# Kernel tuning notes

Hardware: AMD Instinct MI355X
Metric: run time of the kernel (lower is better)

The kernel has to match this reference:

```python
import jax, jax.numpy as jnp
import numpy as np

B, S, D, H = 4, 2048, 1024, 16
HD = D // H  # 64


def setup_inputs() -> dict:
    key = jax.random.key(0)
    ks = jax.random.split(key, 11)
    scale = 1.0 / np.sqrt(D)
    inp = {
        "query": jax.random.normal(ks[0], (B, S, D), jnp.float32),
        "key": jax.random.normal(ks[1], (B, S, D), jnp.float32),
        "value": jax.random.normal(ks[2], (B, S, D), jnp.float32),
        "mask": jnp.ones((B, 1, 1, S), jnp.float32),
        "wq": jax.random.normal(ks[3], (D, D), jnp.float32) * scale,
        "bq": jnp.zeros((D,), jnp.float32),
        "wk": jax.random.normal(ks[4], (D, D), jnp.float32) * scale,
        "bk": jnp.zeros((D,), jnp.float32),
        "wv": jax.random.normal(ks[5], (D, D), jnp.float32) * scale,
        "bv": jnp.zeros((D,), jnp.float32),
        "wo": jax.random.normal(ks[6], (D, D), jnp.float32) * scale,
        "bo": jnp.zeros((D,), jnp.float32),
    }
    return inp


def reference(query, key, value, mask, wq, bq, wk, bk, wv, bv, wo, bo):
    b = query.shape[0]
    # Dense QKV projections
    q = query @ wq + bq  # [B,S,D]
    k = key @ wk + bk
    v = value @ wv + bv

    def split_heads(x):
        return x.reshape(b, -1, H, HD).transpose(0, 2, 1, 3)  # [B,H,S,HD]

    q, k, v = split_heads(q), split_heads(k), split_heads(v)
    score = jnp.einsum("bhqd,bhkd->bhqk", q, k) / jnp.sqrt(jnp.float32(HD))
    score = score + (1.0 - mask) * -1e9
    alpha = jax.nn.softmax(score, axis=-1)
    context = jnp.einsum("bhqk,bhkd->bhqd", alpha, v)  # [B,H,S,HD]
    context = context.transpose(0, 2, 1, 3).reshape(b, -1, D)
    return context @ wo + bo
```

## Files before the change

kernel.cpp:

```cpp
#include <hip/hip_runtime.h>

using u16 = unsigned short;
using u32 = unsigned int;

typedef float  f32x4  __attribute__((ext_vector_type(4)));
typedef float  f32x16 __attribute__((ext_vector_type(16)));
typedef u32    u32x4  __attribute__((ext_vector_type(4)));
typedef _Float16 f16;
typedef f16 f16x8 __attribute__((ext_vector_type(8)));

#define DEVI static __device__ __forceinline__

constexpr int S_  = 2048;
constexpr int D_  = 1024;
constexpr int HD_ = 64;
constexpr int SH_ = S_*HD_;
constexpr size_t NE_ = 8192ull*1024ull;

DEVI f32x4 mfma16f(f16x8 a, f16x8 b, f32x4 c){
  return __builtin_amdgcn_mfma_f32_16x16x32_f16(a, b, c, 0, 0, 0);
}
DEVI f32x16 mfma32(f16x8 a, f16x8 b, f32x16 c){
  return __builtin_amdgcn_mfma_f32_32x32x16_f16(a, b, c, 0, 0, 0);
}
DEVI float exp2fast(float x){
#if __has_builtin(__builtin_amdgcn_exp2f)
  return __builtin_amdgcn_exp2f(x);
#else
  float r; asm("v_exp_f32 %0, %1" : "=v"(r) : "v"(x)); return r;
#endif
}
DEVI float rcpfast(float x){
#if __has_builtin(__builtin_amdgcn_rcpf)
  return __builtin_amdgcn_rcpf(x);
#else
  float r; asm("v_rcp_f32 %0, %1" : "=v"(r) : "v"(x)); return r;
#endif
}
DEVI u32 pkh(float a, float b){
  return __builtin_bit_cast(u32, __builtin_amdgcn_cvt_pkrtz(a, b));
}
DEVI void gld16(const void* g, void* l){
  __builtin_amdgcn_global_load_lds(
      (const __attribute__((address_space(1))) u32*)g,
      (__attribute__((address_space(3))) u32*)l, 16, 0, 0);
}
DEVI void gld4(const void* g, void* l){
  __builtin_amdgcn_global_load_lds(
      (const __attribute__((address_space(1))) u32*)g,
      (__attribute__((address_space(3))) u32*)l, 4, 0, 0);
}

__global__ __launch_bounds__(256) void wcvt_k(
    const float* __restrict__ wq, const float* __restrict__ wk,
    const float* __restrict__ wv, const float* __restrict__ wo,
    u16* __restrict__ wt)
{
  int z = blockIdx.z;
  const float* W = (z==0)?wq:(z==1)?wk:(z==2)?wv:wo;
  u16* ot = wt + (size_t)z*D_*D_;
  __shared__ float t[64][65];
  int k0 = blockIdx.y*64, n0 = blockIdx.x*64;
  int tid = threadIdx.x;
#pragma unroll
  for (int i=0;i<4;i++){
    int lin = i*256 + tid;
    int r = lin>>4, c = (lin&15)*4;
    f32x4 v = *reinterpret_cast<const f32x4*>(W + (size_t)(k0+r)*D_ + n0 + c);
    t[r][c+0]=v.x; t[r][c+1]=v.y; t[r][c+2]=v.z; t[r][c+3]=v.w;
  }
  __syncthreads();
  int n = tid>>2, c0 = (tid&3)*16;
  alignas(16) u16 hb[16];
#pragma unroll
  for (int i=0;i<16;i++) hb[i] = __builtin_bit_cast(u16, (f16)t[c0+i][n]);
  size_t off = (size_t)(n0+n)*D_ + k0 + c0;
  *reinterpret_cast<u32x4*>(ot+off)   = *reinterpret_cast<u32x4*>(hb);
  *reinterpret_cast<u32x4*>(ot+off+8) = *reinterpret_cast<u32x4*>(hb+8);
}

__global__ __launch_bounds__(256) void acvt_k(
    const float* __restrict__ q, const float* __restrict__ k,
    const float* __restrict__ v, u16* __restrict__ out)
{
  int z = blockIdx.y;
  const float* src = (z==0)?q:(z==1)?k:v;
  u16* dst = out + (size_t)z*NE_;
  size_t i = ((size_t)blockIdx.x*256 + threadIdx.x)*8;
  f32x4 a = *reinterpret_cast<const f32x4*>(src + i);
  f32x4 b = *reinterpret_cast<const f32x4*>(src + i + 4);
  u32x4 t;
  t.x = pkh(a.x,a.y); t.y = pkh(a.z,a.w);
  t.z = pkh(b.x,b.y); t.w = pkh(b.z,b.w);
  *reinterpret_cast<u32x4*>(dst + i) = t;
}

__global__ __launch_bounds__(256) void madd_k(const float* __restrict__ mask,
                                              float* __restrict__ madd2)
{
  int i = blockIdx.x*256 + threadIdx.x;
  if (i < 4*S_) madd2[i] = (1.0f - mask[i]) * -1442695040.0f;
}

struct GemmArgs {
  const void* A[3];
  const u16*  Wt[3];
  const float* bias[3];
  float*      outF[3];
  u16*        outH[3];
  float       scale[3];
  int         mode[3];
};

__global__ __launch_bounds__(512, 4) void gemm_k(GemmArgs args)
{
  int z = blockIdx.z;
  const u16*   __restrict__ A    = (const u16*)args.A[z];
  const u16*   __restrict__ Wt   = args.Wt[z];
  const float* __restrict__ bias = args.bias[z];
  int mode = args.mode[z];
  float sc = args.scale[z];

  constexpr int ABYT = 16384;
  constexpr int BUFS = ABYT + 8192;
  __shared__ __align__(16) unsigned char smem[73728];
  char* sbase = (char*)smem;

  int m0 = blockIdx.x*256, n0 = blockIdx.y*128;
  int tid = threadIdx.x, lane = tid&63, w = tid>>6;
  int wm = (w>>1)*64, wn = (w&1)*64;
  int lr = lane&15, lh = lane>>4;

  int offA[2], offB;
#pragma unroll
  for (int j=0;j<2;j++){
    int chunk = w*2 + j;
    int row = chunk*16 + (lane>>2);
    int gs = lane&3;
    offA[j] = row*D_ + (((gs - (row>>1)) & 3)*8);
  }
  {
    int row = w*16 + (lane>>2);
    int gs = lane&3;
    offB = row*D_ + (((gs - (row>>1)) & 3)*8);
  }

  f32x4 acc[4][4];
#pragma unroll
  for (int m=0;m<4;m++)
#pragma unroll
    for (int n=0;n<4;n++) acc[m][n] = f32x4{0.f,0.f,0.f,0.f};

  auto STAGE = [&](int buf, int kt){
    char* lA = sbase + buf*BUFS;
    char* lB = lA + ABYT;
    const u16* As = A  + (size_t)m0*D_ + kt*32;
#pragma unroll
    for (int j=0;j<2;j++) gld16(As + offA[j], lA + (w*2+j)*1024);
    const u16* Bs = Wt + (size_t)n0*D_ + kt*32;
    gld16(Bs + offB, lB + w*1024);
  };

  STAGE(0, 0);
  STAGE(1, 1);
  STAGE(2, 2);

  for (int kt=0; kt<32; ++kt){
    int buf = kt - (kt/3)*3;
    if (kt < 30)       asm volatile("s_waitcnt vmcnt(6)" ::: "memory");
    else if (kt == 30) asm volatile("s_waitcnt vmcnt(3)" ::: "memory");
    else               asm volatile("s_waitcnt vmcnt(0)" ::: "memory");
    __builtin_amdgcn_s_barrier();

    char* bA = sbase + buf*BUFS;
    char* bB = bA + ABYT;
    f16x8 af[4], bfr[4];
#pragma unroll
    for (int m=0;m<4;m++){
      int row = wm + m*16 + lr;
      af[m] = *reinterpret_cast<const f16x8*>(bA + row*64 + (((lh + (row>>1)) & 3)<<4));
    }
#pragma unroll
    for (int n=0;n<4;n++){
      int row = wn + n*16 + lr;
      bfr[n] = *reinterpret_cast<const f16x8*>(bB + row*64 + (((lh + (row>>1)) & 3)<<4));
    }
    asm volatile("s_waitcnt lgkmcnt(0)" ::: "memory");
    __builtin_amdgcn_sched_barrier(0);
    __builtin_amdgcn_s_barrier();
    if (kt < 29) STAGE(buf, kt+3);

    __builtin_amdgcn_s_setprio(1);
#pragma unroll
    for (int m=0;m<4;m++)
#pragma unroll
      for (int n=0;n<4;n++)
        acc[m][n] = mfma16f(af[m], bfr[n], acc[m][n]);
    __builtin_amdgcn_s_setprio(0);
  }

  float bsetv[4];
#pragma unroll
  for (int n=0;n<4;n++) bsetv[n] = bias[n0 + wn + n*16 + lr];

  if (mode == 0){
    float* out = args.outF[z];
#pragma unroll
    for (int m=0;m<4;m++)
#pragma unroll
      for (int n=0;n<4;n++)
#pragma unroll
        for (int r=0;r<4;r++){
          int row = m0 + wm + m*16 + lh*4 + r;
          int col = n0 + wn + n*16 + lr;
          out[(size_t)row*D_ + col] = (acc[m][n][r] + bsetv[n])*sc;
        }
  } else if (mode == 1){
    u16* oh = args.outH[z];
#pragma unroll
    for (int m=0;m<4;m++)
#pragma unroll
      for (int n=0;n<4;n++)
#pragma unroll
        for (int r=0;r<4;r++){
          int row = m0 + wm + m*16 + lh*4 + r;
          int col = n0 + wn + n*16 + lr;
          float val = (acc[m][n][r] + bsetv[n])*sc;
          int b = row >> 11, s = row & 2047;
          int hh = col >> 6,  dd = col & 63;
          oh[(size_t)(b*16 + hh)*SH_ + (size_t)s*HD_ + dd] =
              __builtin_bit_cast(u16, (f16)val);
        }
  } else {
    __syncthreads();
    u16* ct = (u16*)sbase;
#pragma unroll
    for (int m=0;m<4;m++)
#pragma unroll
      for (int n=0;n<4;n++)
#pragma unroll
        for (int r=0;r<4;r++){
          int lrow = wm + m*16 + lh*4 + r;
          int lcol = wn + n*16 + lr;
          ct[lrow*132 + lcol] = __builtin_bit_cast(u16, (f16)((acc[m][n][r] + bsetv[n])*sc));
        }
    __syncthreads();
    u16* ovt = args.outH[z];
    int b = m0 >> 11, s0 = m0 & 2047;
    int ch = tid >> 2, quarter = tid & 3;
    int gn = n0 + ch;
    int hh = gn >> 6, dd = gn & 63;
    size_t obase = (size_t)(b*16 + hh)*SH_ + (size_t)dd*S_ + s0 + quarter*64;
#pragma unroll
    for (int i=0;i<8;i++){
      alignas(16) u16 tmp[8];
#pragma unroll
      for (int j=0;j<8;j++) tmp[j] = ct[(quarter*64 + i*8 + j)*132 + ch];
      *reinterpret_cast<u32x4*>(ovt + obase + i*8) = *reinterpret_cast<u32x4*>(tmp);
    }
  }
}

__global__ __launch_bounds__(256, 2) void attn_k(
    const f16* __restrict__ Qf, const f16* __restrict__ Kf,
    const f16* __restrict__ Vt, const float* __restrict__ madd2,
    u16* __restrict__ cf)
{
  constexpr int BUFS = 16640;
  __shared__ __align__(16) unsigned char smem[3*BUFS];
  char* sbase = (char*)smem;

  int flat = blockIdx.x + blockIdx.y*gridDim.x;
  int xcd = flat & 7, ix = flat >> 3;
  int bh = xcd + 8*(ix >> 4);
  int qx = ix & 15;
  int b = bh >> 4, head = bh & 15;

  const f16* Qb = Qf + (size_t)bh*SH_;
  const f16* Kb = Kf + (size_t)bh*SH_;
  const f16* Vb = Vt + (size_t)bh*SH_;
  const float* mb = madd2 + (size_t)b*S_;

  int tid = threadIdx.x, lane = tid&63, w = tid>>6;
  int q31 = lane&31, h = lane>>5;
  int qw = qx*128 + w*32;
  int xorv = (q31&7)<<4;

  f16x8 qb[4];
#pragma unroll
  for (int ks=0;ks<4;ks++)
    qb[ks] = *reinterpret_cast<const f16x8*>(Qb + (size_t)(qw + q31)*HD_ + ks*16 + h*8);

  int offK[2], offV[2];
#pragma unroll
  for (int j=0;j<2;j++){
    int L = (w*2+j)*1024 + lane*16;
    int r = L>>7;
    int dby = (L&127) ^ ((r&7)<<4);
    offK[j] = r*HD_ + (dby>>1);
    offV[j] = r*S_  + (dby>>1);
  }

  u32 one2 = 0x3C003C00u;
  u32x4 onev; onev.x=one2; onev.y=one2; onev.z=one2; onev.w=one2;
  f16x8 vones = __builtin_bit_cast(f16x8, onev);

  f32x16 o[2], ol;
#pragma unroll
  for (int n=0;n<2;n++)
#pragma unroll
    for (int r=0;r<16;r++) o[n][r] = 0.f;
#pragma unroll
  for (int r=0;r<16;r++) ol[r] = 0.f;

  auto STAGE = [&](int buf, int kt){
    int kv0 = kt*64;
    char* sKb = sbase + buf*BUFS;
    char* sVb = sKb + 8192;
    char* sMb = sKb + 16384;
#pragma unroll
    for (int j=0;j<2;j++)
      gld16(Kb + (size_t)kv0*HD_ + offK[j], sKb + (w*2+j)*1024);
#pragma unroll
    for (int j=0;j<2;j++)
      gld16(Vb + kv0 + offV[j], sVb + (w*2+j)*1024);
    gld4(mb + kv0 + lane, sMb);
  };

  STAGE(0, 0);
  STAGE(1, 1);
  STAGE(2, 2);

  for (int kt=0; kt<32; ++kt){
    int buf = kt - (kt/3)*3;
    char* sKb = sbase + buf*BUFS;
    char* sVb = sKb + 8192;
    float* sMb = (float*)(sKb + 16384);

    if (kt < 30)       asm volatile("s_waitcnt vmcnt(10)" ::: "memory");
    else if (kt == 30) asm volatile("s_waitcnt vmcnt(5)"  ::: "memory");
    else               asm volatile("s_waitcnt vmcnt(0)"  ::: "memory");
    __builtin_amdgcn_s_barrier();
    __builtin_amdgcn_sched_barrier(0);

    f32x16 st[2];
#pragma unroll
    for (int n=0;n<2;n++)
#pragma unroll
      for (int r=0;r<16;r++) st[n][r] = 0.f;

    __builtin_amdgcn_s_setprio(1);
#pragma unroll
    for (int n=0;n<2;n++){
      int rb = (n*32 + q31)*128;
#pragma unroll
      for (int ks=0;ks<4;ks++){
        f16x8 ka = *reinterpret_cast<const f16x8*>(sKb + ((rb + ks*32 + h*16) ^ xorv));
        st[n] = mfma32(ka, qb[ks], st[n]);
      }
    }
    __builtin_amdgcn_s_setprio(0);

    float mval = sMb[lane];
    if (__ballot(mval != 0.0f)){
#pragma unroll
      for (int n=0;n<2;n++)
#pragma unroll
        for (int g=0;g<4;g++){
          f32x4 mv = *reinterpret_cast<const f32x4*>(sMb + n*32 + g*8 + h*4);
#pragma unroll
          for (int c=0;c<4;c++) st[n][g*4+c] += mv[c];
        }
    }

#pragma unroll
    for (int n=0;n<2;n++)
#pragma unroll
      for (int r=0;r<16;r++) st[n][r] = exp2fast(st[n][r]);

    f16x8 pa[4];
#pragma unroll
    for (int n=0;n<2;n++){
      u32 x[4], y[4];
#pragma unroll
      for (int T=0;T<4;T++){
        x[T] = pkh(st[n][4*T+0], st[n][4*T+1]);
        y[T] = pkh(st[n][4*T+2], st[n][4*T+3]);
      }
#pragma unroll
      for (int k2=0;k2<2;k2++){
        u32 a0=x[2*k2], b0=x[2*k2+1], a1=y[2*k2], b1=y[2*k2+1];
        asm volatile("v_permlane32_swap_b32 %0, %1" : "+v"(a0), "+v"(b0));
        asm volatile("v_permlane32_swap_b32 %0, %1" : "+v"(a1), "+v"(b1));
        u32x4 wv;
        wv.x = a0;
        wv.y = a1;
        wv.z = b0;
        wv.w = b1;
        pa[2*n+k2] = __builtin_bit_cast(f16x8, wv);
      }
    }

    __builtin_amdgcn_s_setprio(1);
#pragma unroll
    for (int n=0;n<2;n++){
      int rb = (n*32 + q31)*128;
#pragma unroll
      for (int ks=0;ks<4;ks++){
        f16x8 vbf = *reinterpret_cast<const f16x8*>(sVb + ((rb + ks*32 + h*16) ^ xorv));
        o[n] = mfma32(pa[ks], vbf, o[n]);
      }
    }
#pragma unroll
    for (int ks=0;ks<4;ks++)
      ol = mfma32(pa[ks], vones, ol);
    __builtin_amdgcn_s_setprio(0);

    asm volatile("s_waitcnt lgkmcnt(0)" ::: "memory");
    __builtin_amdgcn_s_barrier();
    __builtin_amdgcn_sched_barrier(0);
    if (kt < 29) STAGE(buf, kt+3);
  }

#pragma unroll
  for (int n=0;n<2;n++)
#pragma unroll
    for (int r=0;r<16;r++){
      float inv = rcpfast(ol[r]);
      int s = qw + (r&3) + 8*(r>>2) + 4*h;
      int d = head*HD_ + n*32 + q31;
      cf[((size_t)(b*S_ + s))*D_ + d] = __builtin_bit_cast(u16, (f16)(o[n][r]*inv));
    }
}

extern "C" void kernel_launch(void* const* d_in, const int* in_sizes, int n_in,
                              void* d_out, int out_size, void* d_ws, size_t ws_size,
                              hipStream_t stream)
{
  (void)in_sizes; (void)n_in; (void)out_size;
  const float* query=(const float*)d_in[0];
  const float* key  =(const float*)d_in[1];
  const float* value=(const float*)d_in[2];
  const float* mask =(const float*)d_in[3];
  const float* wq=(const float*)d_in[4];
  const float* bq=(const float*)d_in[5];
  const float* wk=(const float*)d_in[6];
  const float* bk=(const float*)d_in[7];
  const float* wv=(const float*)d_in[8];
  const float* bv=(const float*)d_in[9];
  const float* wo=(const float*)d_in[10];
  const float* bo=(const float*)d_in[11];
  float* out = (float*)d_out;

  const size_t WN = 4ull*1024*1024;
  size_t need = WN*2 + 3*NE_*2 + 3*NE_*2 + NE_*2 + 8192*4;
  if (ws_size < need) return;

  char* ws = (char*)d_ws;
  u16* wt = (u16*)ws;
  u16* aq = wt + WN;
  u16* ak = aq + NE_;
  u16* av = ak + NE_;
  u16* qf = av + NE_;
  u16* kf = qf + NE_;
  u16* vt = kf + NE_;
  u16* cf = vt + NE_;
  float* madd2 = (float*)(cf + NE_);

  const float CSC = 0.18033688011112042f;

  wcvt_k<<<dim3(16,16,4), 256, 0, stream>>>(wq,wk,wv,wo,wt);
  acvt_k<<<dim3(4096,3), 256, 0, stream>>>(query,key,value,aq);
  madd_k<<<dim3(32), 256, 0, stream>>>(mask, madd2);

  GemmArgs ga{};
  ga.A[0]=aq; ga.A[1]=ak; ga.A[2]=av;
  ga.Wt[0]=wt;           ga.Wt[1]=wt+1048576;   ga.Wt[2]=wt+2097152;
  ga.bias[0]=bq; ga.bias[1]=bk; ga.bias[2]=bv;
  ga.scale[0]=CSC; ga.scale[1]=1.0f; ga.scale[2]=1.0f;
  ga.mode[0]=1;  ga.mode[1]=1;  ga.mode[2]=2;
  ga.outH[0]=qf; ga.outH[1]=kf; ga.outH[2]=vt;
  gemm_k<<<dim3(32,8,3), 512, 0, stream>>>(ga);

  attn_k<<<dim3(16,64), 256, 0, stream>>>((const f16*)qf,(const f16*)kf,(const f16*)vt,madd2,cf);

  GemmArgs go{};
  go.A[0]=cf;
  go.Wt[0]=wt+3145728;
  go.bias[0]=bo; go.scale[0]=1.0f; go.mode[0]=0; go.outF[0]=out;
  gemm_k<<<dim3(32,8,1), 512, 0, stream>>>(go);
}
```

Before: 213.7 us.

## Software-pipeline QK^T of next KV tile with softmax/PV of current tile

```diff
diff --git a/kernel.cpp b/kernel.cpp
--- a/kernel.cpp
+++ b/kernel.cpp
@@ -305,6 +305,10 @@
   u32x4 onev; onev.x=one2; onev.y=one2; onev.z=one2; onev.w=one2;
   f16x8 vones = __builtin_bit_cast(f16x8, onev);
 
+  f32x16 z16;
+#pragma unroll
+  for (int r=0;r<16;r++) z16[r] = 0.f;
+
   f32x16 o[2], ol;
 #pragma unroll
   for (int n=0;n<2;n++)
@@ -327,39 +331,36 @@
     gld4(mb + kv0 + lane, sMb);
   };
 
-  STAGE(0, 0);
-  STAGE(1, 1);
-  STAGE(2, 2);
-
-  for (int kt=0; kt<32; ++kt){
-    int buf = kt - (kt/3)*3;
-    char* sKb = sbase + buf*BUFS;
-    char* sVb = sKb + 8192;
-    float* sMb = (float*)(sKb + 16384);
-
-    if (kt < 30)       asm volatile("s_waitcnt vmcnt(10)" ::: "memory");
-    else if (kt == 30) asm volatile("s_waitcnt vmcnt(5)"  ::: "memory");
-    else               asm volatile("s_waitcnt vmcnt(0)"  ::: "memory");
-    __builtin_amdgcn_s_barrier();
-    __builtin_amdgcn_sched_barrier(0);
-
-    f32x16 st[2];
-#pragma unroll
-    for (int n=0;n<2;n++)
-#pragma unroll
-      for (int r=0;r<16;r++) st[n][r] = 0.f;
-
+  auto QK = [&](char* sKb, f32x16 (&st)[2]){
     __builtin_amdgcn_s_setprio(1);
 #pragma unroll
     for (int n=0;n<2;n++){
       int rb = (n*32 + q31)*128;
-#pragma unroll
-      for (int ks=0;ks<4;ks++){
+      f16x8 k0 = *reinterpret_cast<const f16x8*>(sKb + ((rb + h*16) ^ xorv));
+      st[n] = mfma32(k0, qb[0], z16);
+#pragma unroll
+      for (int ks=1;ks<4;ks++){
         f16x8 ka = *reinterpret_cast<const f16x8*>(sKb + ((rb + ks*32 + h*16) ^ xorv));
         st[n] = mfma32(ka, qb[ks], st[n]);
       }
     }
     __builtin_amdgcn_s_setprio(0);
+  };
+
+  auto TILE = [&](int t, f32x16 (&cur)[2], f32x16 (&nxt)[2], bool qknext){
+    int bt = t - (t/3)*3;
+    int bn = (t+1) - ((t+1)/3)*3;
+    char* sKt = sbase + bt*BUFS;
+    char* sVb = sKt + 8192;
+    float* sMb = (float*)(sKt + 16384);
+    char* sKn = sbase + bn*BUFS;
+
+    if (t < 30) asm volatile("s_waitcnt vmcnt(5)" ::: "memory");
+    else        asm volatile("s_waitcnt vmcnt(0)" ::: "memory");
+    __builtin_amdgcn_s_barrier();
+    __builtin_amdgcn_sched_barrier(0);
+
+    if (qknext) QK(sKn, nxt);
 
     float mval = sMb[lane];
     if (__ballot(mval != 0.0f)){
@@ -369,14 +370,14 @@
         for (int g=0;g<4;g++){
           f32x4 mv = *reinterpret_cast<const f32x4*>(sMb + n*32 + g*8 + h*4);
 #pragma unroll
-          for (int c=0;c<4;c++) st[n][g*4+c] += mv[c];
+          for (int c=0;c<4;c++) cur[n][g*4+c] += mv[c];
         }
     }
 
 #pragma unroll
     for (int n=0;n<2;n++)
 #pragma unroll
-      for (int r=0;r<16;r++) st[n][r] = exp2fast(st[n][r]);
+      for (int r=0;r<16;r++) cur[n][r] = exp2fast(cur[n][r]);
 
     f16x8 pa[4];
 #pragma unroll
@@ -384,8 +385,8 @@
       u32 x[4], y[4];
 #pragma unroll
       for (int T=0;T<4;T++){
-        x[T] = pkh(st[n][4*T+0], st[n][4*T+1]);
-        y[T] = pkh(st[n][4*T+2], st[n][4*T+3]);
+        x[T] = pkh(cur[n][4*T+0], cur[n][4*T+1]);
+        y[T] = pkh(cur[n][4*T+2], cur[n][4*T+3]);
       }
 #pragma unroll
       for (int k2=0;k2<2;k2++){
@@ -419,7 +420,24 @@
     asm volatile("s_waitcnt lgkmcnt(0)" ::: "memory");
     __builtin_amdgcn_s_barrier();
     __builtin_amdgcn_sched_barrier(0);
-    if (kt < 29) STAGE(buf, kt+3);
+    if (t <= 28) STAGE(bt, t+3);
+  };
+
+  f32x16 stA[2], stB[2];
+
+  STAGE(0, 0);
+  STAGE(1, 1);
+  STAGE(2, 2);
+
+  asm volatile("s_waitcnt vmcnt(10)" ::: "memory");
+  __builtin_amdgcn_s_barrier();
+  __builtin_amdgcn_sched_barrier(0);
+  QK(sbase, stA);
+
+  for (int i=0;i<16;++i){
+    int u = 2*i, v = 2*i+1;
+    TILE(u, stA, stB, true);
+    TILE(v, stB, stA, v < 31);
   }
 
 #pragma unroll
```

After: 213.6 us. About the same (-0.1%).

## Double-buffer 128-key tiles in attention loop instead of triple-buffered 64-key tiles

Applied to the files above, without the earlier changes.

```diff
diff --git a/kernel.cpp b/kernel.cpp
--- a/kernel.cpp
+++ b/kernel.cpp
@@ -266,8 +266,8 @@
     const f16* __restrict__ Vt, const float* __restrict__ madd2,
     u16* __restrict__ cf)
 {
-  constexpr int BUFS = 16640;
-  __shared__ __align__(16) unsigned char smem[3*BUFS];
+  constexpr int BUFS = 33280;
+  __shared__ __align__(16) unsigned char smem[2*BUFS];
   char* sbase = (char*)smem;
 
   int flat = blockIdx.x + blockIdx.y*gridDim.x;
@@ -291,20 +291,26 @@
   for (int ks=0;ks<4;ks++)
     qb[ks] = *reinterpret_cast<const f16x8*>(Qb + (size_t)(qw + q31)*HD_ + ks*16 + h*8);
 
-  int offK[2], offV[2];
-#pragma unroll
-  for (int j=0;j<2;j++){
-    int L = (w*2+j)*1024 + lane*16;
-    int r = L>>7;
-    int dby = (L&127) ^ ((r&7)<<4);
-    offK[j] = r*HD_ + (dby>>1);
-    offV[j] = r*S_  + (dby>>1);
+  int offK[4], offV[4];
+#pragma unroll
+  for (int j=0;j<4;j++){
+    int L = (w*4+j)*1024 + lane*16;
+    int rK = L>>7;
+    int dbyK = (L&127) ^ ((rK&7)<<4);
+    offK[j] = rK*HD_ + (dbyK>>1);
+    int rV = L>>8;
+    int dbyV = (L&255) ^ ((rV&7)<<4);
+    offV[j] = rV*S_ + (dbyV>>1);
   }
 
   u32 one2 = 0x3C003C00u;
   u32x4 onev; onev.x=one2; onev.y=one2; onev.z=one2; onev.w=one2;
   f16x8 vones = __builtin_bit_cast(f16x8, onev);
 
+  f32x16 z16;
+#pragma unroll
+  for (int r=0;r<16;r++) z16[r] = 0.f;
+
   f32x16 o[2], ol;
 #pragma unroll
   for (int n=0;n<2;n++)
@@ -313,113 +319,125 @@
 #pragma unroll
   for (int r=0;r<16;r++) ol[r] = 0.f;
 
-  auto STAGE = [&](int buf, int kt){
-    int kv0 = kt*64;
+  auto STAGE = [&](int buf, int t){
+    int kv0 = t*128;
     char* sKb = sbase + buf*BUFS;
-    char* sVb = sKb + 8192;
-    char* sMb = sKb + 16384;
-#pragma unroll
-    for (int j=0;j<2;j++)
-      gld16(Kb + (size_t)kv0*HD_ + offK[j], sKb + (w*2+j)*1024);
-#pragma unroll
-    for (int j=0;j<2;j++)
-      gld16(Vb + kv0 + offV[j], sVb + (w*2+j)*1024);
+    char* sVb = sKb + 16384;
+    char* sMb = sKb + 32768;
+#pragma unroll
+    for (int j=0;j<4;j++)
+      gld16(Kb + (size_t)kv0*HD_ + offK[j], sKb + (w*4+j)*1024);
+#pragma unroll
+    for (int j=0;j<4;j++)
+      gld16(Vb + kv0 + offV[j], sVb + (w*4+j)*1024);
     gld4(mb + kv0 + lane, sMb);
+    gld4(mb + kv0 + 64 + lane, sMb + 256);
   };
 
   STAGE(0, 0);
   STAGE(1, 1);
-  STAGE(2, 2);
-
-  for (int kt=0; kt<32; ++kt){
-    int buf = kt - (kt/3)*3;
+
+  for (int t=0; t<16; ++t){
+    int buf = t&1;
     char* sKb = sbase + buf*BUFS;
-    char* sVb = sKb + 8192;
-    float* sMb = (float*)(sKb + 16384);
-
-    if (kt < 30)       asm volatile("s_waitcnt vmcnt(10)" ::: "memory");
-    else if (kt == 30) asm volatile("s_waitcnt vmcnt(5)"  ::: "memory");
-    else               asm volatile("s_waitcnt vmcnt(0)"  ::: "memory");
+    char* sVb = sKb + 16384;
+    float* sMb = (float*)(sKb + 32768);
+
+    if (t < 15) asm volatile("s_waitcnt vmcnt(10)" ::: "memory");
+    else        asm volatile("s_waitcnt vmcnt(0)"  ::: "memory");
     __builtin_amdgcn_s_barrier();
     __builtin_amdgcn_sched_barrier(0);
 
-    f32x16 st[2];
-#pragma unroll
-    for (int n=0;n<2;n++)
-#pragma unroll
-      for (int r=0;r<16;r++) st[n][r] = 0.f;
+    f32x16 stA[2], stB[2];
 
     __builtin_amdgcn_s_setprio(1);
 #pragma unroll
     for (int n=0;n<2;n++){
       int rb = (n*32 + q31)*128;
-#pragma unroll
-      for (int ks=0;ks<4;ks++){
-        f16x8 ka = *reinterpret_cast<const f16x8*>(sKb + ((rb + ks*32 + h*16) ^ xorv));
-        st[n] = mfma32(ka, qb[ks], st[n]);
+      f16x8 ka = *reinterpret_cast<const f16x8*>(sKb + ((rb + h*16) ^ xorv));
+      stA[n] = mfma32(ka, qb[0], z16);
+#pragma unroll
+      for (int ks=1;ks<4;ks++){
+        ka = *reinterpret_cast<const f16x8*>(sKb + ((rb + ks*32 + h*16) ^ xorv));
+        stA[n] = mfma32(ka, qb[ks], stA[n]);
+      }
+    }
+#pragma unroll
+    for (int n=0;n<2;n++){
+      int rb = (64 + n*32 + q31)*128;
+      f16x8 ka = *reinterpret_cast<const f16x8*>(sKb + ((rb + h*16) ^ xorv));
+      stB[n] = mfma32(ka, qb[0], z16);
+#pragma unroll
+      for (int ks=1;ks<4;ks++){
+        ka = *reinterpret_cast<const f16x8*>(sKb + ((rb + ks*32 + h*16) ^ xorv));
+        stB[n] = mfma32(ka, qb[ks], stB[n]);
       }
     }
     __builtin_amdgcn_s_setprio(0);
 
-    float mval = sMb[lane];
-    if (__ballot(mval != 0.0f)){
+    auto SMPV = [&](int sub, f32x16 (&st)[2]){
+      float mval = sMb[sub*64 + lane];
+      if (__ballot(mval != 0.0f)){
+#pragma unroll
+        for (int n=0;n<2;n++)
+#pragma unroll
+          for (int g=0;g<4;g++){
+            f32x4 mv = *reinterpret_cast<const f32x4*>(sMb + sub*64 + n*32 + g*8 + h*4);
+#pragma unroll
+            for (int c=0;c<4;c++) st[n][g*4+c] += mv[c];
+          }
+      }
 #pragma unroll
       for (int n=0;n<2;n++)
 #pragma unroll
-        for (int g=0;g<4;g++){
-          f32x4 mv = *reinterpret_cast<const f32x4*>(sMb + n*32 + g*8 + h*4);
-#pragma unroll
-          for (int c=0;c<4;c++) st[n][g*4+c] += mv[c];
+        for (int r=0;r<16;r++) st[n][r] = exp2fast(st[n][r]);
+
+      f16x8 pa[4];
+#pragma unroll
+      for (int n=0;n<2;n++){
+        u32 x[4], y[4];
+#pragma unroll
+        for (int T=0;T<4;T++){
+          x[T] = pkh(st[n][4*T+0], st[n][4*T+1]);
+          y[T] = pkh(st[n][4*T+2], st[n][4*T+3]);
         }
-    }
-
-#pragma unroll
-    for (int n=0;n<2;n++)
-#pragma unroll
-      for (int r=0;r<16;r++) st[n][r] = exp2fast(st[n][r]);
-
-    f16x8 pa[4];
-#pragma unroll
-    for (int n=0;n<2;n++){
-      u32 x[4], y[4];
-#pragma unroll
-      for (int T=0;T<4;T++){
-        x[T] = pkh(st[n][4*T+0], st[n][4*T+1]);
-        y[T] = pkh(st[n][4*T+2], st[n][4*T+3]);
+#pragma unroll
+        for (int k2=0;k2<2;k2++){
+          u32 a0=x[2*k2], b0=x[2*k2+1], a1=y[2*k2], b1=y[2*k2+1];
+          asm volatile("v_permlane32_swap_b32 %0, %1" : "+v"(a0), "+v"(b0));
+          asm volatile("v_permlane32_swap_b32 %0, %1" : "+v"(a1), "+v"(b1));
+          u32x4 wv;
+          wv.x = a0;
+          wv.y = a1;
+          wv.z = b0;
+          wv.w = b1;
+          pa[2*n+k2] = __builtin_bit_cast(f16x8, wv);
+        }
       }
-#pragma unroll
-      for (int k2=0;k2<2;k2++){
-        u32 a0=x[2*k2], b0=x[2*k2+1], a1=y[2*k2], b1=y[2*k2+1];
-        asm volatile("v_permlane32_swap_b32 %0, %1" : "+v"(a0), "+v"(b0));
-        asm volatile("v_permlane32_swap_b32 %0, %1" : "+v"(a1), "+v"(b1));
-        u32x4 wv;
-        wv.x = a0;
-        wv.y = a1;
-        wv.z = b0;
-        wv.w = b1;
-        pa[2*n+k2] = __builtin_bit_cast(f16x8, wv);
+
+      __builtin_amdgcn_s_setprio(1);
+#pragma unroll
+      for (int n=0;n<2;n++){
+        int rbv = (n*32 + q31)*256 + sub*128;
+#pragma unroll
+        for (int ks=0;ks<4;ks++){
+          f16x8 vbf = *reinterpret_cast<const f16x8*>(sVb + ((rbv + ks*32 + h*16) ^ xorv));
+          o[n] = mfma32(pa[ks], vbf, o[n]);
+        }
       }
-    }
-
-    __builtin_amdgcn_s_setprio(1);
-#pragma unroll
-    for (int n=0;n<2;n++){
-      int rb = (n*32 + q31)*128;
-#pragma unroll
-      for (int ks=0;ks<4;ks++){
-        f16x8 vbf = *reinterpret_cast<const f16x8*>(sVb + ((rb + ks*32 + h*16) ^ xorv));
-        o[n] = mfma32(pa[ks], vbf, o[n]);
-      }
-    }
-#pragma unroll
-    for (int ks=0;ks<4;ks++)
-      ol = mfma32(pa[ks], vones, ol);
-    __builtin_amdgcn_s_setprio(0);
+#pragma unroll
+      for (int ks=0;ks<4;ks++)
+        ol = mfma32(pa[ks], vones, ol);
+      __builtin_amdgcn_s_setprio(0);
+    };
+
+    SMPV(0, stA);
+    SMPV(1, stB);
 
     asm volatile("s_waitcnt lgkmcnt(0)" ::: "memory");
     __builtin_amdgcn_s_barrier();
     __builtin_amdgcn_sched_barrier(0);
-    if (kt < 29) STAGE(buf, kt+3);
+    if (t < 14) STAGE(buf, t+2);
   }
 
 #pragma unroll
```

Result: no change. 211.3 us (-1.1%).
